# Kernel optimization log

Measured on AMD Instinct MI355X. Metric: run time of the kernel, lower is better.

Reference implementation:

```python
import jax, jax.numpy as jnp
import numpy as np

DIM1 = 128; DIM3 = 256; SCALE = 8; DEPTH = 12
RADIUS = 4; NUM_LEVELS = 4; WIN = 2 * RADIUS + 1
HID = 324 + DIM1          # 452 GRU hidden channels
CIN = HID + DIM1          # 580 conv input channels
B = 2; IMG_H = 256; IMG_W = 512
H = IMG_H // SCALE; W = IMG_W // SCALE  # 32, 64


def conv2d(x, w, b, pad):
    y = jax.lax.conv_general_dilated(x, w, (1, 1), pad,
                                     dimension_numbers=('NCHW', 'OIHW', 'NCHW'))
    return y + b[None, :, None, None]


def bilinear_sample(img, coords):
    # img: (C, Hc, Wc); coords: (..., 2) = (x, y) pixel coords; zero padding
    # (equivalent to F.grid_sample(..., align_corners=True) in RAFT)
    C, Hc, Wc = img.shape
    x, y = coords[..., 0], coords[..., 1]
    x0 = jnp.floor(x); y0 = jnp.floor(y)
    wx1 = x - x0; wx0 = 1.0 - wx1
    wy1 = y - y0; wy0 = 1.0 - wy1

    def tap(xi, yi, wgt):
        valid = (xi >= 0) & (xi <= Wc - 1) & (yi >= 0) & (yi <= Hc - 1)
        xc = jnp.clip(xi.astype(jnp.int32), 0, Wc - 1)
        yc = jnp.clip(yi.astype(jnp.int32), 0, Hc - 1)
        return img[:, yc, xc] * (wgt * valid)[None]

    return (tap(x0, y0, wx0 * wy0) + tap(x0 + 1.0, y0, wx1 * wy0)
            + tap(x0, y0 + 1.0, wx0 * wy1) + tap(x0 + 1.0, y0 + 1.0, wx1 * wy1))


def corr_lookup(fmap1, fmap2, coords):
    # RAFT CorrBlock: full all-pairs correlation pyramid + (2r+1)^2 window lookup
    Bn, C, Hh, Ww = fmap1.shape
    corr = jnp.einsum('bcn,bcm->bnm',
                      fmap1.reshape(Bn, C, Hh * Ww),
                      fmap2.reshape(Bn, C, Hh * Ww)) / jnp.sqrt(jnp.float32(C))
    pyr = corr.reshape(Bn * Hh * Ww, 1, Hh, Ww)
    d = jnp.arange(-RADIUS, RADIUS + 1, dtype=jnp.float32)
    cx = coords[:, 0].reshape(-1)   # (B*H*W,) x pixel coords
    cy = coords[:, 1].reshape(-1)
    N = Bn * Hh * Ww
    outs = []
    for lvl in range(NUM_LEVELS):
        sx = cx / (2 ** lvl); sy = cy / (2 ** lvl)
        # RAFT quirk: x-offset varies along window dim 0, y-offset along dim 1
        ox = jnp.broadcast_to(sx[:, None, None] + d[None, :, None], (N, WIN, WIN))
        oy = jnp.broadcast_to(sy[:, None, None] + d[None, None, :], (N, WIN, WIN))
        cl = jnp.stack([ox, oy], axis=-1)                 # (N, 9, 9, 2)
        sampled = jax.vmap(bilinear_sample)(pyr, cl)      # (N, 1, 9, 9)
        outs.append(sampled.reshape(Bn, Hh, Ww, -1))
        n, c, hl, wl = pyr.shape
        pyr = pyr.reshape(n, c, hl // 2, 2, wl // 2, 2).mean(axis=(3, 5))  # avg_pool2d(2,2)
    return jnp.concatenate(outs, axis=-1).transpose(0, 3, 1, 2)  # (B, 324, H, W)


def gru_step(h, xin, params):
    wz1, bz1, wr1, br1, wq1, bq1, wz2, bz2, wr2, br2, wq2, bq2 = params
    p15 = ((0, 0), (2, 2)); p51 = ((2, 2), (0, 0))
    hx = jnp.concatenate([h, xin], axis=1)
    z = jax.nn.sigmoid(conv2d(hx, wz1, bz1, p15))
    r = jax.nn.sigmoid(conv2d(hx, wr1, br1, p15))
    q = jnp.tanh(conv2d(jnp.concatenate([r * h, xin], axis=1), wq1, bq1, p15))
    h = (1.0 - z) * h + z * q
    hx = jnp.concatenate([h, xin], axis=1)
    z = jax.nn.sigmoid(conv2d(hx, wz2, bz2, p51))
    r = jax.nn.sigmoid(conv2d(hx, wr2, br2, p51))
    q = jnp.tanh(conv2d(jnp.concatenate([r * h, xin], axis=1), wq2, bq2, p51))
    return (1.0 - z) * h + z * q


def setup_inputs() -> dict:
    key = jax.random.key(0)
    ks = jax.random.split(key, 17)
    w = lambda k, s: jax.random.normal(k, s, dtype=jnp.float32) * 0.02
    return {
        'x': jax.random.normal(ks[0], (B * 2, H, W, 2 * DIM1), dtype=jnp.float32),
        'image1': jax.random.normal(ks[1], (B, 3, IMG_H, IMG_W), dtype=jnp.float32),
        'i_ana': 0,
        'wz1': w(ks[2], (HID, CIN, 1, 5)), 'bz1': w(ks[3], (HID,)),
        'wr1': w(ks[4], (HID, CIN, 1, 5)), 'br1': w(ks[5], (HID,)),
        'wq1': w(ks[6], (HID, CIN, 1, 5)), 'bq1': w(ks[7], (HID,)),
        'wz2': w(ks[8], (HID, CIN, 5, 1)), 'bz2': w(ks[9], (HID,)),
        'wr2': w(ks[10], (HID, CIN, 5, 1)), 'br2': w(ks[11], (HID,)),
        'wq2': w(ks[12], (HID, CIN, 5, 1)), 'bq2': w(ks[13], (HID,)),
        'wc': w(ks[14], (DIM3, HID, 3, 3)), 'bc': w(ks[15], (DIM3,)),
    }


def reference(x, image1, i_ana, wz1, bz1, wr1, br1, wq1, bq1,
              wz2, bz2, wr2, br2, wq2, bq2, wc, bc):
    Bt = image1.shape[0]
    feat = x.reshape(Bt, 2, H, W, 2 * DIM1)
    fmap1 = feat[:, 0].transpose(0, 3, 1, 2)   # (B, 2*dim1, H, W)
    fmap2 = feat[:, 1].transpose(0, 3, 1, 2)
    net = jnp.tanh(fmap1[:, :DIM1])
    inp = jax.nn.relu(fmap1[:, DIM1:])
    # coords_grid: (B, 2, H, W) with channel 0 = x, channel 1 = y
    gx, gy = jnp.meshgrid(jnp.arange(W, dtype=jnp.float32),
                          jnp.arange(H, dtype=jnp.float32), indexing='xy')
    coords = jnp.broadcast_to(jnp.stack([gx, gy], axis=0)[None], (Bt, 2, H, W))
    corr = corr_lookup(fmap1, fmap2, coords)   # (B, 324, H, W)
    net = jnp.concatenate([corr, net], axis=1)  # (B, 452, H, W)
    params = (wz1, bz1, wr1, br1, wq1, bq1, wz2, bz2, wr2, br2, wq2, bq2)
    for _ in range(DEPTH):
        net = gru_step(net, inp, params)
    out = jax.nn.relu(conv2d(net, wc, bc, ((1, 1), (1, 1))))
    b, c, h2, w2 = out.shape
    return out.reshape(b, c, h2 // 2, 2, w2 // 2, 2).mean(axis=(3, 5))  # AvgPool2d(2,2)
```

## Files before the change

### kernel.cpp

```cpp
#include <hip/hip_runtime.h>
#include <hip/hip_bf16.h>
#include <cstdint>

#define DEV static __device__ __forceinline__

typedef short bf16x8 __attribute__((ext_vector_type(8)));
typedef float f32x4 __attribute__((ext_vector_type(4)));

constexpr size_t CORR0_OFF = 0;
constexpr size_t LVL1_OFF  = CORR0_OFF + 33554432ull;
constexpr size_t LVL2_OFF  = LVL1_OFF  + 8388608ull;
constexpr size_t LVL3_OFF  = LVL2_OFF  + 2097152ull;
constexpr size_t F1_OFF    = LVL3_OFF  + 524288ull;
constexpr size_t F2_OFF    = F1_OFF    + 2097152ull;
constexpr size_t INP_OFF   = F2_OFF    + 2097152ull;
constexpr size_t HF_OFF    = INP_OFF   + 1048576ull;
constexpr size_t HB_OFF    = HF_OFF    + 8388608ull;
constexpr size_t RH_OFF    = HB_OFF    + 4194304ull;
constexpr size_t Z_OFF     = RH_OFF    + 4194304ull;
constexpr size_t CP1_OFF   = Z_OFF     + 8388608ull;
constexpr size_t CP2_OFF   = CP1_OFF   + 25165824ull;
constexpr size_t WA1_OFF   = CP2_OFF   + 25165824ull;
constexpr size_t WA2_OFF   = WA1_OFF   + 5242880ull;
constexpr size_t WB1_OFF   = WA2_OFF   + 5242880ull;
constexpr size_t WB2_OFF   = WB1_OFF   + 2621440ull;
constexpr size_t WI1_OFF   = WB2_OFF   + 2621440ull;
constexpr size_t WI2_OFF   = WI1_OFF   + 1966080ull;
constexpr size_t WFIN_OFF  = WI2_OFF   + 1966080ull;
constexpr size_t OP_OFF    = WFIN_OFF  + 2359296ull;
constexpr size_t ZP_OFF    = OP_OFF    + 4194304ull;

DEV unsigned short f2bf(float f) {
  unsigned int u = __float_as_uint(f);
  u += 0x7fffu + ((u >> 16) & 1u);
  return (unsigned short)(u >> 16);
}
DEV float bf2f(unsigned short u) { return __uint_as_float(((unsigned)u) << 16); }

DEV void gload16(const void* src, void* dst) {
  __builtin_amdgcn_global_load_lds(
      (const __attribute__((address_space(1))) void*)src,
      (__attribute__((address_space(3))) void*)dst, 16, 0, 0);
}

__launch_bounds__(256)
__global__ void prep_kernel(const float* __restrict__ x, unsigned short* f1, unsigned short* f2,
                            float* h_f32, unsigned short* h_b16, unsigned short* inp, float* zp) {
  int bx = blockIdx.x;
  int s = bx >> 11, n = bx & 2047, c = (int)threadIdx.x;
  float v = x[((size_t)(s * 2048 + n)) * 256 + c];
  int b = s >> 1;
  unsigned short bv = f2bf(v);
  size_t p = (size_t)b * 2048 + n;
  if (s & 1) {
    f2[p * 256 + c] = bv;
  } else {
    f1[p * 256 + c] = bv;
    if (c < 128) {
      float tv = tanhf(v);
      h_f32[p * 512 + 324 + c] = tv;
      h_b16[p * 512 + 324 + c] = f2bf(tv);
    } else {
      float rv = fmaxf(v, 0.f);
      inp[p * 128 + (c - 128)] = f2bf(rv);
    }
    if (c < 60) { h_f32[p * 512 + 452 + c] = 0.f; h_b16[p * 512 + 452 + c] = 0; }
  }
  if (bx == 0) zp[c] = 0.f;
}

__launch_bounds__(256)
__global__ void wprep_kernel(const float* s0, const float* s1, const float* s2,
                             unsigned short* dst, int TK, int K, int Kvalid, int icOff,
                             int sOC, int sIC) {
  long idx = (long)blockIdx.x * 256 + threadIdx.x;
  int n = (int)(idx / TK);
  int rem = (int)(idx % TK);
  int t = rem / K, k = rem % K;
  int sec = n >> 9, ocl = n & 511;
  const float* sp = (sec == 0) ? s0 : (sec == 1 ? s1 : s2);
  float v = 0.f;
  if (ocl < 452 && k < Kvalid) v = sp[(size_t)ocl * sOC + (size_t)(icOff + k) * sIC + t];
  dst[idx] = f2bf(v);
}

__launch_bounds__(256)
__global__ void pyr_kernel(const float* __restrict__ corr0, float* l1, float* l2, float* l3) {
  __shared__ float s0[2048];
  __shared__ float s1[512];
  __shared__ float s2[128];
  int bn = blockIdx.x, tid = (int)threadIdx.x;
  const float4* src = (const float4*)(corr0 + (size_t)bn * 2048);
  ((float4*)s0)[tid] = src[tid];
  ((float4*)s0)[tid + 256] = src[tid + 256];
  __syncthreads();
  for (int o = tid; o < 512; o += 256) {
    int yy = o >> 5, xx = o & 31;
    float v = 0.25f * (s0[(yy*2)*64 + xx*2] + s0[(yy*2)*64 + xx*2 + 1] +
                       s0[(yy*2+1)*64 + xx*2] + s0[(yy*2+1)*64 + xx*2 + 1]);
    s1[o] = v; l1[(size_t)bn * 512 + o] = v;
  }
  __syncthreads();
  if (tid < 128) {
    int yy = tid >> 4, xx = tid & 15;
    float v = 0.25f * (s1[(yy*2)*32 + xx*2] + s1[(yy*2)*32 + xx*2 + 1] +
                       s1[(yy*2+1)*32 + xx*2] + s1[(yy*2+1)*32 + xx*2 + 1]);
    s2[tid] = v; l2[(size_t)bn * 128 + tid] = v;
  }
  __syncthreads();
  if (tid < 32) {
    int yy = tid >> 3, xx = tid & 7;
    float v = 0.25f * (s2[(yy*2)*16 + xx*2] + s2[(yy*2)*16 + xx*2 + 1] +
                       s2[(yy*2+1)*16 + xx*2] + s2[(yy*2+1)*16 + xx*2 + 1]);
    l3[(size_t)bn * 32 + tid] = v;
  }
}

__launch_bounds__(256)
__global__ void lookup_kernel(const float* __restrict__ corr0, const float* __restrict__ l1,
                              const float* __restrict__ l2, const float* __restrict__ l3,
                              float* h_f32, unsigned short* h_b16) {
  __shared__ float s0[2048];
  __shared__ float s1[512];
  __shared__ float s2[128];
  __shared__ float s3[32];
  int bn = blockIdx.x, tid = (int)threadIdx.x;
  ((float4*)s0)[tid] = ((const float4*)(corr0 + (size_t)bn * 2048))[tid];
  ((float4*)s0)[tid + 256] = ((const float4*)(corr0 + (size_t)bn * 2048))[tid + 256];
  if (tid < 128) ((float4*)s1)[tid] = ((const float4*)(l1 + (size_t)bn * 512))[tid];
  if (tid < 32)  ((float4*)s2)[tid] = ((const float4*)(l2 + (size_t)bn * 128))[tid];
  if (tid < 8)   ((float4*)s3)[tid] = ((const float4*)(l3 + (size_t)bn * 32))[tid];
  __syncthreads();
  int x = bn & 63, y = (bn >> 6) & 31;
  for (int ch = tid; ch < 324; ch += 256) {
    int lvl = ch / 81, w = ch % 81;
    int di = w / 9 - 4, dj = w % 9 - 4;
    const float* sl = (lvl == 0) ? s0 : (lvl == 1) ? s1 : (lvl == 2) ? s2 : s3;
    int wl = 64 >> lvl, hl = 32 >> lvl;
    float sx = (float)x / (float)(1 << lvl) + (float)di;
    float sy = (float)y / (float)(1 << lvl) + (float)dj;
    float fx0 = floorf(sx), fy0 = floorf(sy);
    int x0 = (int)fx0, y0 = (int)fy0;
    float wx1 = sx - fx0, wx0 = 1.f - wx1;
    float wy1 = sy - fy0, wy0 = 1.f - wy1;
    float acc = 0.f;
    if (x0 >= 0 && x0 < wl && y0 >= 0 && y0 < hl)         acc += sl[y0*wl + x0] * wx0 * wy0;
    if (x0+1 >= 0 && x0+1 < wl && y0 >= 0 && y0 < hl)     acc += sl[y0*wl + x0+1] * wx1 * wy0;
    if (x0 >= 0 && x0 < wl && y0+1 >= 0 && y0+1 < hl)     acc += sl[(y0+1)*wl + x0] * wx0 * wy1;
    if (x0+1 >= 0 && x0+1 < wl && y0+1 >= 0 && y0+1 < hl) acc += sl[(y0+1)*wl + x0+1] * wx1 * wy1;
    h_f32[(size_t)bn * 512 + ch] = acc;
    h_b16[(size_t)bn * 512 + ch] = f2bf(acc);
  }
}

constexpr int KN = 0, KH = 1, KV = 2, KF = 3;
constexpr int EC = 0, EP = 1, EA = 2, EB = 3, EF = 4;

struct GArgs {
  const char* A; int AstrB; long AbatchB;
  const char* B; int KelB;  long BbatchB;
  const float* e0; const float* e1; const float* e2;
  const unsigned short* b0;
  float* f0; unsigned short* u0;
  long CbatchE;
  const char* zp;
};

template<int MT, int KIND, int TAPS>
DEV void stage_act(const char* Ab, int AstrB, char* ldsbuf, int t, int ckOff, int p0, const char* zp) {
  #pragma unroll
  for (int it = 0; it < (MT * 8) / 256; ++it) {
    int gi = it * 256 + (int)threadIdx.x;
    int row = gi >> 3, gs = gi & 7;
    int gl = gs ^ (row & 7);
    int p = p0 + row;
    bool valid = true; int sh = 0;
    const char* src = valid ? (Ab + (size_t)(p + sh) * (size_t)AstrB + ckOff + gl * 16)
                            : (zp + gl * 16);
    char* dst = ldsbuf + ((size_t)(it * 256 + ((int)threadIdx.x & ~63)) * 16);
    gload16(src, dst);
  }
}

template<int NT, int TAPS>
DEV void stage_w(const char* Bb, int KelB, char* ldsbuf, int t, int ckOff, int n0) {
  #pragma unroll
  for (int it = 0; it < (NT * 8) / 256; ++it) {
    int gi = it * 256 + (int)threadIdx.x;
    int row = gi >> 3, gs = gi & 7;
    int gl = gs ^ (row & 7);
    int n = n0 + row;
    const char* src = Bb + ((size_t)n * TAPS + t) * (size_t)KelB + ckOff + gl * 16;
    char* dst = ldsbuf + ((size_t)(it * 256 + ((int)threadIdx.x & ~63)) * 16);
    gload16(src, dst);
  }
}

template<int Mf, int Nf, int WM, int WN>
DEV void compute_chunk(const char* lA, const char* lB, f32x4 acc[Mf][Nf], int wm, int wn) {
  const int lane = (int)threadIdx.x & 63;
  const int l15 = lane & 15, g = lane >> 4;
  #pragma unroll
  for (int ks = 0; ks < 2; ++ks) {
    bf16x8 a[Mf], b[Nf];
    int q = ks * 4 + g;
    #pragma unroll
    for (int mf = 0; mf < Mf; ++mf) {
      int r = wm * WM + mf * 16 + l15;
      a[mf] = *(const bf16x8*)(lA + r * 128 + ((q ^ (r & 7)) * 16));
    }
    #pragma unroll
    for (int nf = 0; nf < Nf; ++nf) {
      int r = wn * WN + nf * 16 + l15;
      b[nf] = *(const bf16x8*)(lB + r * 128 + ((q ^ (r & 7)) * 16));
    }
    #pragma unroll
    for (int mf = 0; mf < Mf; ++mf)
      #pragma unroll
      for (int nf = 0; nf < Nf; ++nf)
        acc[mf][nf] = __builtin_amdgcn_mfma_f32_16x16x32_bf16(a[mf], b[nf], acc[mf][nf], 0, 0, 0);
  }
}

template<int EPI>
DEV void epilogue_store(const GArgs& g, float v, int p, int ng, int bz) {
  if constexpr (EPI == EC) {
    g.f0[(size_t)bz * (size_t)g.CbatchE + (size_t)p * 2048 + ng] = v * 0.0625f;
  } else if constexpr (EPI == EP) {
    float bias;
    if (ng < 512)       bias = (ng < 452) ? g.e0[ng] : 0.f;
    else if (ng < 1024) bias = (ng - 512 < 452) ? g.e1[ng - 512] : 0.f;
    else                bias = (ng - 1024 < 452) ? g.e2[ng - 1024] : 0.f;
    g.u0[(size_t)p * 1536 + ng] = f2bf(v + bias);
  } else if constexpr (EPI == EA) {
    float pre = v + bf2f(g.b0[(size_t)p * 1536 + ng]);
    float s = 1.f / (1.f + __expf(-pre));
    if (ng < 512) {
      g.f0[(size_t)p * 512 + ng] = s;
    } else {
      int oc = ng - 512;
      float rh = s * g.e1[(size_t)p * 512 + oc];
      g.u0[(size_t)p * 512 + oc] = f2bf(rh);
    }
  } else if constexpr (EPI == EB) {
    float pre = v + bf2f(g.b0[(size_t)p * 1536 + 1024 + ng]);
    float e = __expf(-2.f * fabsf(pre));
    float tt = (1.f - e) / (1.f + e);
    float qv = (pre < 0.f) ? -tt : tt;
    float z = g.e1[(size_t)p * 512 + ng];
    float ho = g.e2[(size_t)p * 512 + ng];
    float hn = (1.f - z) * ho + z * qv;
    g.f0[(size_t)p * 512 + ng] = hn;
    g.u0[(size_t)p * 512 + ng] = f2bf(hn);
  } else {
    float r = fmaxf(v + g.e0[ng], 0.f);
    g.f0[(size_t)p * 256 + ng] = r;
  }
}

template<int MT, int NT, int WSM, int EPI, int CPT, int MINB>
__launch_bounds__(256, MINB)
__global__ void kgemm(GArgs g) {
  constexpr int WSN = 4 / WSM;
  constexpr int WM = MT / WSM, WN = NT / WSN, Mf = WM / 16, Nf = WN / 16;
  constexpr int BUFB = (MT + NT) * 128;
  __shared__ __attribute__((aligned(16))) char lds[2 * BUFB];
  const int p0 = blockIdx.x * MT, n0 = blockIdx.y * NT;
  const int bz = blockIdx.z;
  const char* Ab = g.A + (size_t)bz * (size_t)g.AbatchB;
  const char* Bb = g.B + (size_t)bz * (size_t)g.BbatchB;
  const int wave = (int)threadIdx.x >> 6;
  const int wm = wave / WSN, wn = wave % WSN;
  f32x4 acc[Mf][Nf] = {};

  auto do_stage = [&](int buf, int c) {
    char* base = lds + (size_t)buf * BUFB;
    stage_act<MT, KN, 1>(Ab, g.AstrB, base, 0, c * 128, p0, g.zp);
    stage_w<NT, 1>(Bb, g.KelB, base + MT * 128, 0, c * 128, n0);
  };

  do_stage(0, 0);
  asm volatile("s_waitcnt vmcnt(0)" ::: "memory");
  __builtin_amdgcn_s_barrier();
  asm volatile("" ::: "memory");

  #pragma unroll 1
  for (int c = 0; c < CPT; ++c) {
    int cur = c & 1;
    if (c + 1 < CPT) do_stage(cur ^ 1, c + 1);
    const char* base = lds + (size_t)cur * BUFB;
    compute_chunk<Mf, Nf, WM, WN>(base, base + MT * 128, acc, wm, wn);
    asm volatile("s_waitcnt vmcnt(0)" ::: "memory");
    __builtin_amdgcn_s_barrier();
    asm volatile("" ::: "memory");
  }

  const int lane = (int)threadIdx.x & 63;
  const int l15 = lane & 15, gq = lane >> 4;
  #pragma unroll
  for (int mf = 0; mf < Mf; ++mf)
    #pragma unroll
    for (int nf = 0; nf < Nf; ++nf)
      #pragma unroll
      for (int j = 0; j < 4; ++j) {
        int p = p0 + wm * WM + mf * 16 + gq * 4 + j;
        int ng = n0 + wn * WN + nf * 16 + l15;
        epilogue_store<EPI>(g, acc[mf][nf][j], p, ng, bz);
      }
}

template<int MT, int NT, int KIND, int EPI, int TAPS, int CPT, int MINB>
__launch_bounds__(256, MINB)
__global__ void tgemm(GArgs g) {
  constexpr int Gsz = (KIND == KV) ? 32 : 64;
  constexpr int G   = (KIND == KF) ? 3 : MT / Gsz;
  constexpr int S   = (KIND == KF) ? 66 : Gsz + 4;
  constexpr int RA  = G * S;
  constexpr int RAP = (RA + 7) & ~7;
  constexpr int RB  = TAPS * NT;
  constexpr int ITA = (RAP * 8 + 255) / 256;
  constexpr int ITB = (RB * 8 + 255) / 256;
  constexpr int WSN = (NT >= 32) ? 2 : 1;
  constexpr int WSM = 4 / WSN;
  constexpr int WM = MT / WSM, WN = NT / WSN;
  constexpr int Mf = WM / 16, Nf = WN / 16;
  __shared__ __attribute__((aligned(16))) char ldsA[RAP * 128];
  __shared__ __attribute__((aligned(16))) char ldsB[RB * 128];

  const int tid = (int)threadIdx.x;
  const int pg = blockIdx.x * MT;
  const int bz = pg >> 11;
  const int q0 = pg & 2047;
  const int bbase = bz << 11;
  const int n0 = blockIdx.y * NT;
  const char* Ab = g.A + (size_t)bbase * (size_t)g.AstrB;
  const int wave = tid >> 6;
  const int wm = wave / WSN, wn = wave % WSN;
  const int lane = tid & 63;
  const int l15 = lane & 15, gq = lane >> 4;
  f32x4 acc[Mf][Nf] = {};

  auto stageA = [&](int ck) {
    #pragma unroll
    for (int it = 0; it < ITA; ++it) {
      int gi = it * 256 + tid;
      if (ITA * 256 > RAP * 8 && gi >= RAP * 8) continue;
      int sr = gi >> 3, gs = gi & 7;
      int gl = gs ^ (sr & 7);
      bool valid; int gpos;
      if constexpr (KIND == KF) {
        int grp = sr / 66, qq = sr - grp * 66;
        int y = (q0 >> 6) + grp - 1, x = qq - 1;
        valid = (sr < RA) && (qq >= 1) && (qq < 65) && ((unsigned)y < 32u);
        gpos = (y << 6) + x;
      } else {
        int grp = (G == 1) ? 0 : (sr / S);
        int qq = sr - grp * S;
        valid = (sr < RA) && (qq >= 2) && (qq < Gsz + 2);
        int s = q0 + grp * Gsz + (qq - 2);
        if constexpr (KIND == KH) gpos = s;
        else gpos = ((s & 31) << 6) + (s >> 5);
      }
      const char* src = valid ? (Ab + (size_t)gpos * (size_t)g.AstrB + ck * 128 + gl * 16)
                              : (g.zp + gl * 16);
      gload16(src, &ldsA[(size_t)(it * 256 + (tid & ~63)) * 16]);
    }
  };
  auto stageBf = [&](int ck) {
    #pragma unroll
    for (int it = 0; it < ITB; ++it) {
      int gi = it * 256 + tid;
      if (ITB * 256 > RB * 8 && gi >= RB * 8) continue;
      int rb = gi >> 3, gs = gi & 7;
      int gl = gs ^ (rb & 7);
      int t = rb / NT, nl = rb - t * NT;
      const char* src = g.B + ((size_t)(n0 + nl) * TAPS + t) * (size_t)g.KelB + ck * 128 + gl * 16;
      gload16(src, &ldsB[(size_t)(it * 256 + (tid & ~63)) * 16]);
    }
  };

  auto computeC = [&]() {
    #pragma unroll
    for (int t = 0; t < TAPS; ++t) {
      #pragma unroll
      for (int ks = 0; ks < 2; ++ks) {
        int q = ks * 4 + gq;
        bf16x8 a[Mf], b[Nf];
        #pragma unroll
        for (int mf = 0; mf < Mf; ++mf) {
          int m = wm * WM + mf * 16 + l15;
          int r;
          if constexpr (KIND == KF) r = (t / 3) * 66 + (m & 63) + (t % 3);
          else r = (m / Gsz) * S + (m % Gsz) + t;
          a[mf] = *(const bf16x8*)(&ldsA[r * 128 + ((q ^ (r & 7)) * 16)]);
        }
        #pragma unroll
        for (int nf = 0; nf < Nf; ++nf) {
          int rb = t * NT + wn * WN + nf * 16 + l15;
          b[nf] = *(const bf16x8*)(&ldsB[rb * 128 + ((q ^ (rb & 7)) * 16)]);
        }
        #pragma unroll
        for (int mf = 0; mf < Mf; ++mf)
          #pragma unroll
          for (int nf = 0; nf < Nf; ++nf)
            acc[mf][nf] = __builtin_amdgcn_mfma_f32_16x16x32_bf16(a[mf], b[nf], acc[mf][nf], 0, 0, 0);
      }
    }
  };

  stageA(0); stageBf(0);
  asm volatile("s_waitcnt vmcnt(0)" ::: "memory");
  __builtin_amdgcn_s_barrier();
  asm volatile("" ::: "memory");

  #pragma unroll 1
  for (int ck = 0; ck < CPT; ++ck) {
    computeC();
    if (ck + 1 < CPT) {
      asm volatile("" ::: "memory");
      __builtin_amdgcn_s_barrier();
      asm volatile("" ::: "memory");
      stageA(ck + 1); stageBf(ck + 1);
      asm volatile("s_waitcnt vmcnt(0)" ::: "memory");
      __builtin_amdgcn_s_barrier();
      asm volatile("" ::: "memory");
    }
  }

  #pragma unroll
  for (int mf = 0; mf < Mf; ++mf)
    #pragma unroll
    for (int nf = 0; nf < Nf; ++nf)
      #pragma unroll
      for (int j = 0; j < 4; ++j) {
        int m = wm * WM + mf * 16 + gq * 4 + j;
        int s = q0 + m;
        int gpos;
        if constexpr (KIND == KV) gpos = ((s & 31) << 6) + (s >> 5);
        else gpos = s;
        int p = bbase + gpos;
        int ng = n0 + wn * WN + nf * 16 + l15;
        epilogue_store<EPI>(g, acc[mf][nf][j], p, ng, 0);
      }
}

__launch_bounds__(256)
__global__ void pool_kernel(const float* __restrict__ op, float* out) {
  int idx = blockIdx.x * 256 + (int)threadIdx.x;
  int xx = idx & 31, yy = (idx >> 5) & 15, oc = (idx >> 9) & 255, b = idx >> 17;
  size_t p00 = (size_t)b * 2048 + (size_t)(yy * 2) * 64 + xx * 2;
  float v = 0.25f * (op[p00 * 256 + oc] + op[(p00 + 1) * 256 + oc] +
                     op[(p00 + 64) * 256 + oc] + op[(p00 + 65) * 256 + oc]);
  out[idx] = v;
}

extern "C" void kernel_launch(void* const* d_in, const int* in_sizes, int n_in,
                              void* d_out, int out_size, void* d_ws, size_t ws_size,
                              hipStream_t stream) {
  (void)in_sizes; (void)n_in; (void)out_size; (void)ws_size;
  const float* x   = (const float*)d_in[0];
  const float* wz1 = (const float*)d_in[3];  const float* bz1 = (const float*)d_in[4];
  const float* wr1 = (const float*)d_in[5];  const float* br1 = (const float*)d_in[6];
  const float* wq1 = (const float*)d_in[7];  const float* bq1 = (const float*)d_in[8];
  const float* wz2 = (const float*)d_in[9];  const float* bz2 = (const float*)d_in[10];
  const float* wr2 = (const float*)d_in[11]; const float* br2 = (const float*)d_in[12];
  const float* wq2 = (const float*)d_in[13]; const float* bq2 = (const float*)d_in[14];
  const float* wc  = (const float*)d_in[15]; const float* bc  = (const float*)d_in[16];

  char* ws = (char*)d_ws;
  float* corr0 = (float*)(ws + CORR0_OFF);
  float* l1    = (float*)(ws + LVL1_OFF);
  float* l2    = (float*)(ws + LVL2_OFF);
  float* l3    = (float*)(ws + LVL3_OFF);
  unsigned short* f1  = (unsigned short*)(ws + F1_OFF);
  unsigned short* f2p = (unsigned short*)(ws + F2_OFF);
  unsigned short* inp = (unsigned short*)(ws + INP_OFF);
  float* h_f32 = (float*)(ws + HF_OFF);
  unsigned short* h_b16 = (unsigned short*)(ws + HB_OFF);
  unsigned short* rh    = (unsigned short*)(ws + RH_OFF);
  float* zbuf  = (float*)(ws + Z_OFF);
  unsigned short* Cp1 = (unsigned short*)(ws + CP1_OFF);
  unsigned short* Cp2 = (unsigned short*)(ws + CP2_OFF);
  unsigned short* wA1 = (unsigned short*)(ws + WA1_OFF);
  unsigned short* wA2 = (unsigned short*)(ws + WA2_OFF);
  unsigned short* wB1 = (unsigned short*)(ws + WB1_OFF);
  unsigned short* wB2 = (unsigned short*)(ws + WB2_OFF);
  unsigned short* wi1 = (unsigned short*)(ws + WI1_OFF);
  unsigned short* wi2 = (unsigned short*)(ws + WI2_OFF);
  unsigned short* wfn = (unsigned short*)(ws + WFIN_OFF);
  float* outpre = (float*)(ws + OP_OFF);
  float* zp     = (float*)(ws + ZP_OFF);

  prep_kernel<<<8192, 256, 0, stream>>>(x, f1, f2p, h_f32, h_b16, inp, zp);

  wprep_kernel<<<(1024*5*512)/256, 256, 0, stream>>>(wz1, wr1, nullptr, wA1, 5*512, 512, 452, 0, 2900, 5);
  wprep_kernel<<<( 512*5*512)/256, 256, 0, stream>>>(wq1, nullptr, nullptr, wB1, 5*512, 512, 452, 0, 2900, 5);
  wprep_kernel<<<(1536*5*128)/256, 256, 0, stream>>>(wz1, wr1, wq1, wi1, 5*128, 128, 128, 452, 2900, 5);
  wprep_kernel<<<(1024*5*512)/256, 256, 0, stream>>>(wz2, wr2, nullptr, wA2, 5*512, 512, 452, 0, 2900, 5);
  wprep_kernel<<<( 512*5*512)/256, 256, 0, stream>>>(wq2, nullptr, nullptr, wB2, 5*512, 512, 452, 0, 2900, 5);
  wprep_kernel<<<(1536*5*128)/256, 256, 0, stream>>>(wz2, wr2, wq2, wi2, 5*128, 128, 128, 452, 2900, 5);
  wprep_kernel<<<( 256*9*512)/256, 256, 0, stream>>>(wc, nullptr, nullptr, wfn, 9*512, 512, 452, 0, 4068, 9);

  {
    GArgs a = {};
    a.A = (const char*)f1;  a.AstrB = 512; a.AbatchB = 2048L * 512;
    a.B = (const char*)f2p; a.KelB = 512;  a.BbatchB = 2048L * 512;
    a.f0 = corr0; a.CbatchE = 2048L * 2048; a.zp = (const char*)zp;
    kgemm<128,128,2,EC,4,2><<<dim3(16,16,2), 256, 0, stream>>>(a);
  }
  pyr_kernel<<<4096, 256, 0, stream>>>(corr0, l1, l2, l3);
  lookup_kernel<<<4096, 256, 0, stream>>>(corr0, l1, l2, l3, h_f32, h_b16);

  {
    GArgs a = {};
    a.A = (const char*)inp; a.AstrB = 256; a.B = (const char*)wi1; a.KelB = 256;
    a.e0 = bz1; a.e1 = br1; a.e2 = bq1; a.u0 = Cp1; a.zp = (const char*)zp;
    tgemm<64,32,KH,EP,5,2,4><<<dim3(64,48), 256, 0, stream>>>(a);
  }
  {
    GArgs a = {};
    a.A = (const char*)inp; a.AstrB = 256; a.B = (const char*)wi2; a.KelB = 256;
    a.e0 = bz2; a.e1 = br2; a.e2 = bq2; a.u0 = Cp2; a.zp = (const char*)zp;
    tgemm<64,32,KV,EP,5,2,4><<<dim3(64,48), 256, 0, stream>>>(a);
  }

  for (int it = 0; it < 12; ++it) {
    {
      GArgs a = {};
      a.A = (const char*)h_b16; a.AstrB = 1024; a.B = (const char*)wA1; a.KelB = 1024;
      a.b0 = Cp1; a.e1 = h_f32; a.f0 = zbuf; a.u0 = rh; a.zp = (const char*)zp;
      tgemm<128,32,KH,EA,5,8,4><<<dim3(32,32), 256, 0, stream>>>(a);
    }
    {
      GArgs a = {};
      a.A = (const char*)rh; a.AstrB = 1024; a.B = (const char*)wB1; a.KelB = 1024;
      a.b0 = Cp1; a.e1 = zbuf; a.e2 = h_f32; a.f0 = h_f32; a.u0 = h_b16; a.zp = (const char*)zp;
      tgemm<64,32,KH,EB,5,8,4><<<dim3(64,16), 256, 0, stream>>>(a);
    }
    {
      GArgs a = {};
      a.A = (const char*)h_b16; a.AstrB = 1024; a.B = (const char*)wA2; a.KelB = 1024;
      a.b0 = Cp2; a.e1 = h_f32; a.f0 = zbuf; a.u0 = rh; a.zp = (const char*)zp;
      tgemm<128,32,KV,EA,5,8,4><<<dim3(32,32), 256, 0, stream>>>(a);
    }
    {
      GArgs a = {};
      a.A = (const char*)rh; a.AstrB = 1024; a.B = (const char*)wB2; a.KelB = 1024;
      a.b0 = Cp2; a.e1 = zbuf; a.e2 = h_f32; a.f0 = h_f32; a.u0 = h_b16; a.zp = (const char*)zp;
      tgemm<64,32,KV,EB,5,8,4><<<dim3(64,16), 256, 0, stream>>>(a);
    }
  }

  {
    GArgs a = {};
    a.A = (const char*)h_b16; a.AstrB = 1024; a.B = (const char*)wfn; a.KelB = 1024;
    a.e0 = bc; a.f0 = outpre; a.zp = (const char*)zp;
    tgemm<64,16,KF,EF,9,8,3><<<dim3(64,16), 256, 0, stream>>>(a);
  }
  pool_kernel<<<1024, 256, 0, stream>>>(outpre, (float*)d_out);
}
```

Baseline: 1.556 ms.

## Store correlation volume in bf16 and widen tgemm N tiles

The all-pairs correlation GEMM now writes bf16 instead of fp32, and the pyramid and lookup kernels read that bf16 buffer. This halves the traffic of the large corr volume at some precision cost. All tgemm launches double their N tile (32 to 64, 16 to 32 for the final conv) with an explicit warp-split parameter and lower min-blocks, halving grid size to improve weight and activation reuse per block. The staging helpers also drop unused template parameters.

```diff
diff --git a/kernel.cpp b/kernel.cpp
--- a/kernel.cpp
+++ b/kernel.cpp
@@ -6,6 +6,7 @@
 
 typedef short bf16x8 __attribute__((ext_vector_type(8)));
 typedef float f32x4 __attribute__((ext_vector_type(4)));
+typedef unsigned short bfu8 __attribute__((ext_vector_type(8)));
 
 constexpr size_t CORR0_OFF = 0;
 constexpr size_t LVL1_OFF  = CORR0_OFF + 33554432ull;
@@ -85,14 +86,14 @@
 }
 
 __launch_bounds__(256)
-__global__ void pyr_kernel(const float* __restrict__ corr0, float* l1, float* l2, float* l3) {
+__global__ void pyr_kernel(const unsigned short* __restrict__ corr0, float* l1, float* l2, float* l3) {
   __shared__ float s0[2048];
   __shared__ float s1[512];
   __shared__ float s2[128];
   int bn = blockIdx.x, tid = (int)threadIdx.x;
-  const float4* src = (const float4*)(corr0 + (size_t)bn * 2048);
-  ((float4*)s0)[tid] = src[tid];
-  ((float4*)s0)[tid + 256] = src[tid + 256];
+  bfu8 v8 = ((const bfu8*)(corr0 + (size_t)bn * 2048))[tid];
+  #pragma unroll
+  for (int j = 0; j < 8; ++j) s0[tid * 8 + j] = bf2f(v8[j]);
   __syncthreads();
   for (int o = tid; o < 512; o += 256) {
     int yy = o >> 5, xx = o & 31;
@@ -117,7 +118,7 @@
 }
 
 __launch_bounds__(256)
-__global__ void lookup_kernel(const float* __restrict__ corr0, const float* __restrict__ l1,
+__global__ void lookup_kernel(const unsigned short* __restrict__ corr0, const float* __restrict__ l1,
                               const float* __restrict__ l2, const float* __restrict__ l3,
                               float* h_f32, unsigned short* h_b16) {
   __shared__ float s0[2048];
@@ -125,8 +126,9 @@
   __shared__ float s2[128];
   __shared__ float s3[32];
   int bn = blockIdx.x, tid = (int)threadIdx.x;
-  ((float4*)s0)[tid] = ((const float4*)(corr0 + (size_t)bn * 2048))[tid];
-  ((float4*)s0)[tid + 256] = ((const float4*)(corr0 + (size_t)bn * 2048))[tid + 256];
+  bfu8 v8 = ((const bfu8*)(corr0 + (size_t)bn * 2048))[tid];
+  #pragma unroll
+  for (int j = 0; j < 8; ++j) s0[tid * 8 + j] = bf2f(v8[j]);
   if (tid < 128) ((float4*)s1)[tid] = ((const float4*)(l1 + (size_t)bn * 512))[tid];
   if (tid < 32)  ((float4*)s2)[tid] = ((const float4*)(l2 + (size_t)bn * 128))[tid];
   if (tid < 8)   ((float4*)s3)[tid] = ((const float4*)(l3 + (size_t)bn * 32))[tid];
@@ -166,31 +168,29 @@
   const char* zp;
 };
 
-template<int MT, int KIND, int TAPS>
-DEV void stage_act(const char* Ab, int AstrB, char* ldsbuf, int t, int ckOff, int p0, const char* zp) {
+template<int MT>
+DEV void stage_act(const char* Ab, int AstrB, char* ldsbuf, int ckOff, int p0) {
   #pragma unroll
   for (int it = 0; it < (MT * 8) / 256; ++it) {
     int gi = it * 256 + (int)threadIdx.x;
     int row = gi >> 3, gs = gi & 7;
     int gl = gs ^ (row & 7);
     int p = p0 + row;
-    bool valid = true; int sh = 0;
-    const char* src = valid ? (Ab + (size_t)(p + sh) * (size_t)AstrB + ckOff + gl * 16)
-                            : (zp + gl * 16);
+    const char* src = Ab + (size_t)p * (size_t)AstrB + ckOff + gl * 16;
     char* dst = ldsbuf + ((size_t)(it * 256 + ((int)threadIdx.x & ~63)) * 16);
     gload16(src, dst);
   }
 }
 
-template<int NT, int TAPS>
-DEV void stage_w(const char* Bb, int KelB, char* ldsbuf, int t, int ckOff, int n0) {
+template<int NT>
+DEV void stage_wk(const char* Bb, int KelB, char* ldsbuf, int ckOff, int n0) {
   #pragma unroll
   for (int it = 0; it < (NT * 8) / 256; ++it) {
     int gi = it * 256 + (int)threadIdx.x;
     int row = gi >> 3, gs = gi & 7;
     int gl = gs ^ (row & 7);
     int n = n0 + row;
-    const char* src = Bb + ((size_t)n * TAPS + t) * (size_t)KelB + ckOff + gl * 16;
+    const char* src = Bb + (size_t)n * (size_t)KelB + ckOff + gl * 16;
     char* dst = ldsbuf + ((size_t)(it * 256 + ((int)threadIdx.x & ~63)) * 16);
     gload16(src, dst);
   }
@@ -225,7 +225,7 @@
 template<int EPI>
 DEV void epilogue_store(const GArgs& g, float v, int p, int ng, int bz) {
   if constexpr (EPI == EC) {
-    g.f0[(size_t)bz * (size_t)g.CbatchE + (size_t)p * 2048 + ng] = v * 0.0625f;
+    g.u0[(size_t)bz * (size_t)g.CbatchE + (size_t)p * 2048 + ng] = f2bf(v * 0.0625f);
   } else if constexpr (EPI == EP) {
     float bias;
     if (ng < 512)       bias = (ng < 452) ? g.e0[ng] : 0.f;
@@ -275,8 +275,8 @@
 
   auto do_stage = [&](int buf, int c) {
     char* base = lds + (size_t)buf * BUFB;
-    stage_act<MT, KN, 1>(Ab, g.AstrB, base, 0, c * 128, p0, g.zp);
-    stage_w<NT, 1>(Bb, g.KelB, base + MT * 128, 0, c * 128, n0);
+    stage_act<MT>(Ab, g.AstrB, base, c * 128, p0);
+    stage_wk<NT>(Bb, g.KelB, base + MT * 128, c * 128, n0);
   };
 
   do_stage(0, 0);
@@ -309,7 +309,7 @@
       }
 }
 
-template<int MT, int NT, int KIND, int EPI, int TAPS, int CPT, int MINB>
+template<int MT, int NT, int WSM, int KIND, int EPI, int TAPS, int CPT, int MINB>
 __launch_bounds__(256, MINB)
 __global__ void tgemm(GArgs g) {
   constexpr int Gsz = (KIND == KV) ? 32 : 64;
@@ -320,8 +320,7 @@
   constexpr int RB  = TAPS * NT;
   constexpr int ITA = (RAP * 8 + 255) / 256;
   constexpr int ITB = (RB * 8 + 255) / 256;
-  constexpr int WSN = (NT >= 32) ? 2 : 1;
-  constexpr int WSM = 4 / WSN;
+  constexpr int WSN = 4 / WSM;
   constexpr int WM = MT / WSM, WN = NT / WSN;
   constexpr int Mf = WM / 16, Nf = WN / 16;
   __shared__ __attribute__((aligned(16))) char ldsA[RAP * 128];
@@ -468,7 +467,7 @@
   const float* wc  = (const float*)d_in[15]; const float* bc  = (const float*)d_in[16];
 
   char* ws = (char*)d_ws;
-  float* corr0 = (float*)(ws + CORR0_OFF);
+  unsigned short* corr0 = (unsigned short*)(ws + CORR0_OFF);
   float* l1    = (float*)(ws + LVL1_OFF);
   float* l2    = (float*)(ws + LVL2_OFF);
   float* l3    = (float*)(ws + LVL3_OFF);
@@ -505,7 +504,7 @@
     GArgs a = {};
     a.A = (const char*)f1;  a.AstrB = 512; a.AbatchB = 2048L * 512;
     a.B = (const char*)f2p; a.KelB = 512;  a.BbatchB = 2048L * 512;
-    a.f0 = corr0; a.CbatchE = 2048L * 2048; a.zp = (const char*)zp;
+    a.u0 = corr0; a.CbatchE = 2048L * 2048; a.zp = (const char*)zp;
     kgemm<128,128,2,EC,4,2><<<dim3(16,16,2), 256, 0, stream>>>(a);
   }
   pyr_kernel<<<4096, 256, 0, stream>>>(corr0, l1, l2, l3);
@@ -515,13 +514,13 @@
     GArgs a = {};
     a.A = (const char*)inp; a.AstrB = 256; a.B = (const char*)wi1; a.KelB = 256;
     a.e0 = bz1; a.e1 = br1; a.e2 = bq1; a.u0 = Cp1; a.zp = (const char*)zp;
-    tgemm<64,32,KH,EP,5,2,4><<<dim3(64,48), 256, 0, stream>>>(a);
+    tgemm<64,64,2,KH,EP,5,2,2><<<dim3(64,24), 256, 0, stream>>>(a);
   }
   {
     GArgs a = {};
     a.A = (const char*)inp; a.AstrB = 256; a.B = (const char*)wi2; a.KelB = 256;
     a.e0 = bz2; a.e1 = br2; a.e2 = bq2; a.u0 = Cp2; a.zp = (const char*)zp;
-    tgemm<64,32,KV,EP,5,2,4><<<dim3(64,48), 256, 0, stream>>>(a);
+    tgemm<64,64,2,KV,EP,5,2,2><<<dim3(64,24), 256, 0, stream>>>(a);
   }
 
   for (int it = 0; it < 12; ++it) {
@@ -529,25 +528,25 @@
       GArgs a = {};
       a.A = (const char*)h_b16; a.AstrB = 1024; a.B = (const char*)wA1; a.KelB = 1024;
       a.b0 = Cp1; a.e1 = h_f32; a.f0 = zbuf; a.u0 = rh; a.zp = (const char*)zp;
-      tgemm<128,32,KH,EA,5,8,4><<<dim3(32,32), 256, 0, stream>>>(a);
+      tgemm<128,64,2,KH,EA,5,8,2><<<dim3(32,16), 256, 0, stream>>>(a);
     }
     {
       GArgs a = {};
       a.A = (const char*)rh; a.AstrB = 1024; a.B = (const char*)wB1; a.KelB = 1024;
       a.b0 = Cp1; a.e1 = zbuf; a.e2 = h_f32; a.f0 = h_f32; a.u0 = h_b16; a.zp = (const char*)zp;
-      tgemm<64,32,KH,EB,5,8,4><<<dim3(64,16), 256, 0, stream>>>(a);
+      tgemm<64,64,2,KH,EB,5,8,2><<<dim3(64,8), 256, 0, stream>>>(a);
     }
     {
       GArgs a = {};
       a.A = (const char*)h_b16; a.AstrB = 1024; a.B = (const char*)wA2; a.KelB = 1024;
       a.b0 = Cp2; a.e1 = h_f32; a.f0 = zbuf; a.u0 = rh; a.zp = (const char*)zp;
-      tgemm<128,32,KV,EA,5,8,4><<<dim3(32,32), 256, 0, stream>>>(a);
+      tgemm<128,64,2,KV,EA,5,8,2><<<dim3(32,16), 256, 0, stream>>>(a);
     }
     {
       GArgs a = {};
       a.A = (const char*)rh; a.AstrB = 1024; a.B = (const char*)wB2; a.KelB = 1024;
       a.b0 = Cp2; a.e1 = zbuf; a.e2 = h_f32; a.f0 = h_f32; a.u0 = h_b16; a.zp = (const char*)zp;
-      tgemm<64,32,KV,EB,5,8,4><<<dim3(64,16), 256, 0, stream>>>(a);
+      tgemm<64,64,2,KV,EB,5,8,2><<<dim3(64,8), 256, 0, stream>>>(a);
     }
   }
 
@@ -555,7 +554,7 @@
     GArgs a = {};
     a.A = (const char*)h_b16; a.AstrB = 1024; a.B = (const char*)wfn; a.KelB = 1024;
     a.e0 = bc; a.f0 = outpre; a.zp = (const char*)zp;
-    tgemm<64,16,KF,EF,9,8,3><<<dim3(64,16), 256, 0, stream>>>(a);
+    tgemm<64,32,2,KF,EF,9,8,2><<<dim3(64,8), 256, 0, stream>>>(a);
   }
   pool_kernel<<<1024, 256, 0, stream>>>(outpre, (float*)d_out);
 }
```

Result: slower. 1.669 ms (+7.2%).
